# Kernel optimization log

Measured on AMD Instinct MI355X. Metric: run time of the kernel, lower is better.

The kernel has to match this reference:

```python
import jax, jax.numpy as jnp
import numpy as np

DIM = 2048
RANK = 16
NUM_EXPERTS = 8


def setup_inputs() -> dict:
    key = jax.random.key(0)
    ks = jax.random.split(key, 8)
    x = jax.random.normal(ks[0], (4, 2048, DIM), dtype=jnp.float32)
    # router gate: nn.Linear(dim, num_experts) -> weight [E, dim], bias [E]
    gate_w = jax.random.normal(ks[1], (NUM_EXPERTS, DIM), dtype=jnp.float32) * 0.02
    gate_b = jnp.zeros((NUM_EXPERTS,), dtype=jnp.float32)
    # base_ffn: nn.Linear(dim, dim) -> weight [dim, dim], bias [dim]
    base_w = jax.random.normal(ks[2], (DIM, DIM), dtype=jnp.float32) * 0.02
    base_b = jnp.zeros((DIM,), dtype=jnp.float32)
    # LoRA experts, stacked: A maps dim->rank, B maps rank->dim (stored input-major)
    lora_A = jax.random.normal(ks[3], (NUM_EXPERTS, DIM, RANK), dtype=jnp.float32) * 0.02
    lora_B = jax.random.normal(ks[4], (NUM_EXPERTS, RANK, DIM), dtype=jnp.float32) * 0.02
    return {"x": x, "gate_w": gate_w, "gate_b": gate_b,
            "base_w": base_w, "base_b": base_b,
            "lora_A": lora_A, "lora_B": lora_B}


def reference(x, gate_w, gate_b, base_w, base_b, lora_A, lora_B):
    B, S, D = x.shape
    flat = x.reshape(-1, D)  # [T, D]
    # base FFN: Linear + exact GELU (torch default)
    base_out = jax.nn.gelu(flat @ base_w.T + base_b, approximate=False)
    # router: softmax then top-1
    probs = jax.nn.softmax(flat @ gate_w.T + gate_b, axis=-1)  # [T, E]
    idx = jnp.argmax(probs, axis=-1)                            # [T] top-1 index
    w = jnp.take_along_axis(probs, idx[:, None], axis=-1)      # [T, 1] top-1 weight
    E = lora_A.shape[0]
    expert_out = jnp.zeros_like(flat)
    for e in range(E):  # fixed small expert loop; GEMMs are dense over all tokens
        h = jax.nn.gelu(flat @ lora_A[e], approximate=False)   # [T, rank]
        ye = h @ lora_B[e]                                      # [T, D]
        sel = (idx == e)[:, None]
        expert_out = expert_out + jnp.where(sel, ye * w, 0.0)
    out = (base_out + expert_out).reshape(B, S, D)
    return out, probs
```

## Files before the change

### kernel.cpp

```cpp
#include <hip/hip_runtime.h>
#include <hip/hip_bf16.h>
#include <math.h>


#define DIM   2048
#define RANK  16
#define NEXP  8
#define NTOK  8192
#define KLORA 128

typedef __hip_bfloat16 bf16;
typedef __attribute__((ext_vector_type(8))) short short8;
typedef __attribute__((ext_vector_type(4))) float float4v;

typedef const __attribute__((address_space(1))) void* gptr_t;
typedef __attribute__((address_space(3))) void*       sptr_t;

__device__ __forceinline__ void async_ld16(const bf16* g, bf16* l) {
    __builtin_amdgcn_global_load_lds((gptr_t)g, (sptr_t)l, 16, 0, 0);
}

__device__ __forceinline__ float gelu_fast(float x) {
    float t = 0.7978845608028654f * (x + 0.044715f * x * x * x);
    t = fminf(fmaxf(t, -10.0f), 10.0f);
    float e = __expf(2.0f * t);
    float th = (e - 1.0f) / (e + 1.0f);
    return 0.5f * x * (1.0f + th);
}

__device__ __forceinline__ short8 pack8(float4 v0, float4 v1) {
    union { bf16 h[8]; short8 v; } u;
    u.h[0] = __float2bfloat16(v0.x); u.h[1] = __float2bfloat16(v0.y);
    u.h[2] = __float2bfloat16(v0.z); u.h[3] = __float2bfloat16(v0.w);
    u.h[4] = __float2bfloat16(v1.x); u.h[5] = __float2bfloat16(v1.y);
    u.h[6] = __float2bfloat16(v1.z); u.h[7] = __float2bfloat16(v1.w);
    return u.v;
}

__global__ __launch_bounds__(256) void cvt_logits_kernel(
    const float* __restrict__ x, const float* __restrict__ gate_w,
    const float* __restrict__ gate_b, const float* __restrict__ base_w,
    const float* __restrict__ lora_B, const float* __restrict__ lora_A,
    bf16* __restrict__ Xb, bf16* __restrict__ Wb,
    bf16* __restrict__ Bt, bf16* __restrict__ Ab,
    float* __restrict__ probs, int* __restrict__ idx_out, float* __restrict__ w_out)
{
    __shared__ float buf[2560];
    const int b   = blockIdx.x;
    const int tid = threadIdx.x;

    if (b < 1024) {
        const int t0 = b * 8;
        float4 g0[NEXP], g1[NEXP];
        #pragma unroll
        for (int e = 0; e < NEXP; e++) {
            const float* wr = gate_w + (size_t)e * DIM + tid * 8;
            g0[e] = *(const float4*)wr;
            g1[e] = *(const float4*)(wr + 4);
        }
        const int wave = tid >> 6, lane = tid & 63;
        #pragma unroll
        for (int tt = 0; tt < 8; tt++) {
            const int t = t0 + tt;
            const float* xr = x + (size_t)t * DIM + tid * 8;
            float4 v0 = *(const float4*)xr;
            float4 v1 = *(const float4*)(xr + 4);
            *(short8*)(Xb + (size_t)t * DIM + tid * 8) = pack8(v0, v1);
            float a[NEXP];
            #pragma unroll
            for (int e = 0; e < NEXP; e++) {
                a[e] = v0.x * g0[e].x + v0.y * g0[e].y + v0.z * g0[e].z + v0.w * g0[e].w
                     + v1.x * g1[e].x + v1.y * g1[e].y + v1.z * g1[e].z + v1.w * g1[e].w;
                #pragma unroll
                for (int off = 32; off > 0; off >>= 1) a[e] += __shfl_down(a[e], off);
            }
            if (lane == 0) {
                #pragma unroll
                for (int e = 0; e < NEXP; e++) buf[tt * 32 + wave * NEXP + e] = a[e];
            }
        }
        __syncthreads();
        if (tid < 8) {
            const int t = t0 + tid;
            float l[NEXP]; float mx = -1e30f;
            #pragma unroll
            for (int e = 0; e < NEXP; e++) {
                l[e] = buf[tid * 32 + e] + buf[tid * 32 + 8 + e]
                     + buf[tid * 32 + 16 + e] + buf[tid * 32 + 24 + e] + gate_b[e];
                mx = fmaxf(mx, l[e]);
            }
            float sum = 0.f;
            #pragma unroll
            for (int e = 0; e < NEXP; e++) { l[e] = __expf(l[e] - mx); sum += l[e]; }
            float inv = 1.0f / sum;
            int es = 0; float best = l[0];
            #pragma unroll
            for (int e = 1; e < NEXP; e++) if (l[e] > best) { best = l[e]; es = e; }
            #pragma unroll
            for (int e = 0; e < NEXP; e++) probs[(size_t)t * NEXP + e] = l[e] * inv;
            idx_out[t] = es;
            w_out[t]   = best * inv;
        }
    } else if (b < 1024 + 2048) {
        size_t v = ((size_t)(b - 1024) * 256 + tid) * 8;
        float4 v0 = *(const float4*)(base_w + v);
        float4 v1 = *(const float4*)(base_w + v + 4);
        *(short8*)(Wb + v) = pack8(v0, v1);
    } else if (b < 1024 + 2048 + 256) {
        int bb = b - 1024 - 2048;
        int kk0 = (bb >> 6) * 32, j0 = (bb & 63) * 32;
        {
            int r = tid >> 3, c4 = (tid & 7) * 4;
            float4 val = *(const float4*)(lora_B + (size_t)(kk0 + r) * DIM + j0 + c4);
            *(float4*)(buf + r * 36 + c4) = val;
        }
        __syncthreads();
        {
            int j = tid >> 3, k4 = (tid & 7) * 4;
            bf16* dst = Bt + (size_t)(j0 + j) * KLORA + kk0 + k4;
            #pragma unroll
            for (int i = 0; i < 4; i++) dst[i] = __float2bfloat16(buf[(k4 + i) * 36 + j]);
        }
    } else {
        int bb = b - 1024 - 2048 - 256;
        int e = bb >> 4, k0 = (bb & 15) * 128;
        const float* src = lora_A + (size_t)e * DIM * RANK;
        {
            int k = tid >> 2, r4 = (tid & 3) * 4;
            float4 va = *(const float4*)(src + (size_t)(k0 + k) * RANK + r4);
            float4 vb = *(const float4*)(src + (size_t)(k0 + k + 64) * RANK + r4);
            *(float4*)(buf + k * 20 + r4)        = va;
            *(float4*)(buf + (k + 64) * 20 + r4) = vb;
        }
        __syncthreads();
        {
            int r = tid >> 4, kx = (tid & 15) * 8;
            bf16* dst = Ab + (size_t)(e * 16 + r) * DIM + k0 + kx;
            #pragma unroll
            for (int i = 0; i < 8; i++) dst[i] = __float2bfloat16(buf[(kx + i) * 20 + r]);
        }
    }
}

__global__ __launch_bounds__(256) void hsel_kernel(
    const bf16* __restrict__ Xb, const bf16* __restrict__ Ab,
    const int* __restrict__ idx, const float* __restrict__ wsel,
    bf16* __restrict__ A2)
{
    __shared__ bf16 As[32 * 32];
    __shared__ bf16 Bs[64 * 32];
    const int tid  = threadIdx.x;
    const int wave = tid >> 6, lane = tid & 63;
    const int m0 = blockIdx.x * 32;
    const int n0 = blockIdx.y * 64;
    const int col = lane & 15, quad = lane >> 4;

    const int kc = ((tid & 3) ^ ((tid >> 3) & 3)) * 8;
    const bf16* gB = Ab + (size_t)(n0 + (tid >> 2)) * DIM + kc;
    const bf16* gA = Xb + (size_t)(m0 + (tid >> 2)) * DIM + kc;
    bf16* lB = Bs + wave * 512;
    bf16* lA = As + wave * 512;

    const int xr = quad ^ ((col >> 1) & 3);
    const bf16* pa = As + col * 32 + xr * 8;
    const bf16* pb = Bs + (wave * 16 + col) * 32 + xr * 8;

    float4v acc[2] = {};
    for (int k0 = 0; k0 < DIM; k0 += 32) {
        __syncthreads();
        async_ld16(gB + k0, lB);
        if (tid < 128) async_ld16(gA + k0, lA);
        __syncthreads();
        short8 a0 = *(const short8*)pa;
        short8 a1 = *(const short8*)(pa + 512);
        short8 b0 = *(const short8*)pb;
        acc[0] = __builtin_amdgcn_mfma_f32_16x16x32_bf16(a0, b0, acc[0], 0, 0, 0);
        acc[1] = __builtin_amdgcn_mfma_f32_16x16x32_bf16(a1, b0, acc[1], 0, 0, 0);
    }

    const int jcol = n0 + wave * 16 + col;
    const int ej   = jcol >> 4;
    #pragma unroll
    for (int i = 0; i < 2; i++) {
        int rbase = m0 + i * 16 + quad * 4;
        #pragma unroll
        for (int r = 0; r < 4; r++) {
            int t = rbase + r;
            float v = (idx[t] == ej) ? gelu_fast(acc[i][r]) * wsel[t] : 0.0f;
            A2[(size_t)t * KLORA + jcol] = __float2bfloat16(v);
        }
    }
}

__global__ __launch_bounds__(256, 3) void gemm_kernel(
    const bf16* __restrict__ Xb, const bf16* __restrict__ Wb,
    const float* __restrict__ base_b,
    const bf16* __restrict__ A2, const bf16* __restrict__ Bt,
    float* __restrict__ out)
{
    __shared__ bf16 As[128 * 64];
    __shared__ bf16 Bs[128 * 64];
    const int tid  = threadIdx.x;
    const int wave = tid >> 6, lane = tid & 63;
    const int wm = wave >> 1, wn = wave & 1;
    const int n0 = blockIdx.x * 128;
    const int m0 = blockIdx.y * 128;
    const int col = lane & 15, quad = lane >> 4;

    const int kc = (((tid & 7) ^ ((tid >> 3) & 7))) * 8;
    const int r0 = tid >> 3;
    const bf16* gA0 = Xb + (size_t)(m0 + r0) * DIM + kc;
    const bf16* gB0 = Wb + (size_t)(n0 + r0) * DIM + kc;
    const bf16* gA1 = gA0 + (size_t)32 * DIM;
    const bf16* gB1 = gB0 + (size_t)32 * DIM;
    const bf16* gA2 = gA0 + (size_t)64 * DIM;
    const bf16* gB2 = gB0 + (size_t)64 * DIM;
    const bf16* gA3 = gA0 + (size_t)96 * DIM;
    const bf16* gB3 = gB0 + (size_t)96 * DIM;
    bf16* lA = As + wave * 512;
    bf16* lB = Bs + wave * 512;

    const int sl0 = (quad        ^ (col & 7)) * 8;
    const int sl1 = ((quad | 4)  ^ (col & 7)) * 8;
    const bf16* paA = As + (wm * 64 + col) * 64;
    const bf16* pbB = Bs + (wn * 64 + col) * 64;

    float4v acc[4][4] = {};

    for (int k0 = 0; k0 < DIM; k0 += 64) {
        __syncthreads();
        async_ld16(gA0 + k0, lA);
        async_ld16(gA1 + k0, lA + 2048);
        async_ld16(gA2 + k0, lA + 4096);
        async_ld16(gA3 + k0, lA + 6144);
        async_ld16(gB0 + k0, lB);
        async_ld16(gB1 + k0, lB + 2048);
        async_ld16(gB2 + k0, lB + 4096);
        async_ld16(gB3 + k0, lB + 6144);
        __syncthreads();
        {
            short8 a[4], b[4];
            #pragma unroll
            for (int i = 0; i < 4; i++) a[i] = *(const short8*)(paA + i * 1024 + sl0);
            #pragma unroll
            for (int j = 0; j < 4; j++) b[j] = *(const short8*)(pbB + j * 1024 + sl0);
            #pragma unroll
            for (int i = 0; i < 4; i++)
                #pragma unroll
                for (int j = 0; j < 4; j++)
                    acc[i][j] = __builtin_amdgcn_mfma_f32_16x16x32_bf16(
                        a[i], b[j], acc[i][j], 0, 0, 0);
        }
        {
            short8 a[4], b[4];
            #pragma unroll
            for (int i = 0; i < 4; i++) a[i] = *(const short8*)(paA + i * 1024 + sl1);
            #pragma unroll
            for (int j = 0; j < 4; j++) b[j] = *(const short8*)(pbB + j * 1024 + sl1);
            #pragma unroll
            for (int i = 0; i < 4; i++)
                #pragma unroll
                for (int j = 0; j < 4; j++)
                    acc[i][j] = __builtin_amdgcn_mfma_f32_16x16x32_bf16(
                        a[i], b[j], acc[i][j], 0, 0, 0);
        }
    }

    float bias[4];
    #pragma unroll
    for (int j = 0; j < 4; j++) bias[j] = base_b[n0 + wn * 64 + j * 16 + col];
    #pragma unroll
    for (int i = 0; i < 4; i++)
        #pragma unroll
        for (int j = 0; j < 4; j++)
            #pragma unroll
            for (int r = 0; r < 4; r++)
                acc[i][j][r] = gelu_fast(acc[i][j][r] + bias[j]);

    const bf16* pea = A2 + (size_t)(m0 + wm * 64 + col) * KLORA + quad * 8;
    const bf16* peb = Bt + (size_t)(n0 + wn * 64 + col) * KLORA + quad * 8;
    #pragma unroll
    for (int ks = 0; ks < 4; ks++) {
        short8 ea[4], eb[4];
        #pragma unroll
        for (int i = 0; i < 4; i++)
            ea[i] = *(const short8*)(pea + i * 16 * KLORA + ks * 32);
        #pragma unroll
        for (int j = 0; j < 4; j++)
            eb[j] = *(const short8*)(peb + j * 16 * KLORA + ks * 32);
        #pragma unroll
        for (int i = 0; i < 4; i++)
            #pragma unroll
            for (int j = 0; j < 4; j++)
                acc[i][j] = __builtin_amdgcn_mfma_f32_16x16x32_bf16(
                    ea[i], eb[j], acc[i][j], 0, 0, 0);
    }

    #pragma unroll
    for (int i = 0; i < 4; i++) {
        #pragma unroll
        for (int j = 0; j < 4; j++) {
            int tt = m0 + wm * 64 + i * 16 + quad * 4;
            int jj = n0 + wn * 64 + j * 16 + col;
            float* po = out + (size_t)tt * DIM + jj;
            #pragma unroll
            for (int r = 0; r < 4; r++) po[(size_t)r * DIM] = acc[i][j][r];
        }
    }
}

extern "C" void kernel_launch(void* const* d_in, const int* in_sizes, int n_in,
                              void* d_out, int out_size, void* d_ws, size_t ws_size,
                              hipStream_t stream)
{
    (void)in_sizes; (void)n_in; (void)out_size; (void)ws_size;
    const float* x      = (const float*)d_in[0];
    const float* gate_w = (const float*)d_in[1];
    const float* gate_b = (const float*)d_in[2];
    const float* base_w = (const float*)d_in[3];
    const float* base_b = (const float*)d_in[4];
    const float* lora_A = (const float*)d_in[5];
    const float* lora_B = (const float*)d_in[6];

    float* out   = (float*)d_out;
    float* probs = out + (size_t)NTOK * DIM;

    char* ws = (char*)d_ws;
    bf16*  Xb   = (bf16*)ws;
    bf16*  Wb   = (bf16*)(ws + 33554432);
    bf16*  A2   = (bf16*)(ws + 41943040);
    bf16*  Bt   = (bf16*)(ws + 44040192);
    bf16*  Ab   = (bf16*)(ws + 44564480);
    int*   idx  = (int*) (ws + 45088768);
    float* wsel = (float*)(ws + 45121536);

    cvt_logits_kernel<<<1024 + 2048 + 256 + 128, 256, 0, stream>>>(
        x, gate_w, gate_b, base_w, lora_B, lora_A,
        Xb, Wb, Bt, Ab, probs, idx, wsel);
    hsel_kernel<<<dim3(256, 2), 256, 0, stream>>>(Xb, Ab, idx, wsel, A2);
    gemm_kernel<<<dim3(16, 64), 256, 0, stream>>>(Xb, Wb, base_b, A2, Bt, out);
}
```

Baseline: 264.0 us.

## Enlarge GEMM tiles to 256x256 with 4-stage async LDS pipeline

Rewrites the main GEMM as 256x256 tiles with BK=32, 512 threads (8 waves) and a 4-deep ring of LDS buffers. Global-to-LDS async loads are issued three k-steps ahead and paced by explicit vmcnt waits, with MFMA bursts raised in priority via s_setprio. The aim is to hide global memory latency and raise arithmetic intensity per block. In exchange it uses more accumulator registers per wave and launches far fewer blocks (256), which risks poor CU load balance and register spills.

```diff
diff --git a/kernel.cpp b/kernel.cpp
--- a/kernel.cpp
+++ b/kernel.cpp
@@ -8,6 +8,12 @@
 #define NEXP  8
 #define NTOK  8192
 #define KLORA 128
+
+#define BM   256
+#define BN   256
+#define BK   32
+#define NBUF 4
+#define NKT  (DIM / BK)
 
 typedef __hip_bfloat16 bf16;
 typedef __attribute__((ext_vector_type(8))) short short8;
@@ -192,104 +198,126 @@
     }
 }
 
-__global__ __launch_bounds__(256, 3) void gemm_kernel(
+__global__ __launch_bounds__(512, 2) void gemm_kernel(
     const bf16* __restrict__ Xb, const bf16* __restrict__ Wb,
     const float* __restrict__ base_b,
     const bf16* __restrict__ A2, const bf16* __restrict__ Bt,
     float* __restrict__ out)
 {
-    __shared__ bf16 As[128 * 64];
-    __shared__ bf16 Bs[128 * 64];
+    __shared__ bf16 As[NBUF * BM * BK];
+    __shared__ bf16 Bs[NBUF * BN * BK];
     const int tid  = threadIdx.x;
     const int wave = tid >> 6, lane = tid & 63;
-    const int wm = wave >> 1, wn = wave & 1;
-    const int n0 = blockIdx.x * 128;
-    const int m0 = blockIdx.y * 128;
+    const int wm = wave >> 2, wn = wave & 3;
+    const int n0 = blockIdx.x * BN;
+    const int m0 = blockIdx.y * BM;
     const int col = lane & 15, quad = lane >> 4;
 
-    const int kc = (((tid & 7) ^ ((tid >> 3) & 7))) * 8;
-    const int r0 = tid >> 3;
-    const bf16* gA0 = Xb + (size_t)(m0 + r0) * DIM + kc;
-    const bf16* gB0 = Wb + (size_t)(n0 + r0) * DIM + kc;
-    const bf16* gA1 = gA0 + (size_t)32 * DIM;
-    const bf16* gB1 = gB0 + (size_t)32 * DIM;
-    const bf16* gA2 = gA0 + (size_t)64 * DIM;
-    const bf16* gB2 = gB0 + (size_t)64 * DIM;
-    const bf16* gA3 = gA0 + (size_t)96 * DIM;
-    const bf16* gB3 = gB0 + (size_t)96 * DIM;
-    bf16* lA = As + wave * 512;
-    bf16* lB = Bs + wave * 512;
-
-    const int sl0 = (quad        ^ (col & 7)) * 8;
-    const int sl1 = ((quad | 4)  ^ (col & 7)) * 8;
-    const bf16* paA = As + (wm * 64 + col) * 64;
-    const bf16* pbB = Bs + (wn * 64 + col) * 64;
-
-    float4v acc[4][4] = {};
-
-    for (int k0 = 0; k0 < DIM; k0 += 64) {
-        __syncthreads();
-        async_ld16(gA0 + k0, lA);
-        async_ld16(gA1 + k0, lA + 2048);
-        async_ld16(gA2 + k0, lA + 4096);
-        async_ld16(gA3 + k0, lA + 6144);
-        async_ld16(gB0 + k0, lB);
-        async_ld16(gB1 + k0, lB + 2048);
-        async_ld16(gB2 + k0, lB + 4096);
-        async_ld16(gB3 + k0, lB + 6144);
-        __syncthreads();
-        {
-            short8 a[4], b[4];
-            #pragma unroll
-            for (int i = 0; i < 4; i++) a[i] = *(const short8*)(paA + i * 1024 + sl0);
-            #pragma unroll
-            for (int j = 0; j < 4; j++) b[j] = *(const short8*)(pbB + j * 1024 + sl0);
-            #pragma unroll
-            for (int i = 0; i < 4; i++)
-                #pragma unroll
-                for (int j = 0; j < 4; j++)
-                    acc[i][j] = __builtin_amdgcn_mfma_f32_16x16x32_bf16(
-                        a[i], b[j], acc[i][j], 0, 0, 0);
-        }
-        {
-            short8 a[4], b[4];
-            #pragma unroll
-            for (int i = 0; i < 4; i++) a[i] = *(const short8*)(paA + i * 1024 + sl1);
-            #pragma unroll
-            for (int j = 0; j < 4; j++) b[j] = *(const short8*)(pbB + j * 1024 + sl1);
-            #pragma unroll
-            for (int i = 0; i < 4; i++)
-                #pragma unroll
-                for (int j = 0; j < 4; j++)
-                    acc[i][j] = __builtin_amdgcn_mfma_f32_16x16x32_bf16(
-                        a[i], b[j], acc[i][j], 0, 0, 0);
-        }
+    const int kc = ((tid & 3) ^ ((tid >> 3) & 3)) * 8;
+    const int sr = tid >> 2;
+    const bf16* gA = Xb + (size_t)(m0 + sr) * DIM + kc;
+    const bf16* gB = Wb + (size_t)(n0 + sr) * DIM + kc;
+    bf16* lAw = As + wave * 512;
+    bf16* lBw = Bs + wave * 512;
+
+    const int slot = (quad ^ ((col >> 1) & 3)) * 8;
+    const int raoff = (wm * 128 + col) * BK + slot;
+    const int rboff = (wn * 64  + col) * BK + slot;
+
+    float4v acc[8][4] = {};
+
+    #pragma unroll
+    for (int t = 0; t < 3; t++) {
+        const bf16* ga = gA + t * BK;
+        const bf16* gb = gB + t * BK;
+        bf16* la = lAw + t * (BM * BK);
+        bf16* lb = lBw + t * (BN * BK);
+        async_ld16(ga, la);
+        async_ld16(gb, lb);
+        async_ld16(ga + (size_t)128 * DIM, la + 4096);
+        async_ld16(gb + (size_t)128 * DIM, lb + 4096);
+    }
+    asm volatile("s_waitcnt vmcnt(8)" ::: "memory");
+    __builtin_amdgcn_sched_barrier(0);
+    __builtin_amdgcn_s_barrier();
+
+    #pragma unroll 4
+    for (int T = 0; T < NKT; T++) {
+        const int bufc = T & 3;
+        const bf16* pa = As + bufc * (BM * BK) + raoff;
+        const bf16* pb = Bs + bufc * (BN * BK) + rboff;
+        const int ts = T + 3, bufs = ts & 3;
+        const bool st = (ts < NKT);
+        const bf16* gsa = gA + ts * BK;
+        const bf16* gsb = gB + ts * BK;
+        bf16* lsa = lAw + bufs * (BM * BK);
+        bf16* lsb = lBw + bufs * (BN * BK);
+
+        short8 a[4], b[4];
+        #pragma unroll
+        for (int i = 0; i < 4; i++) a[i] = *(const short8*)(pa + i * 16 * BK);
+        #pragma unroll
+        for (int j = 0; j < 4; j++) b[j] = *(const short8*)(pb + j * 16 * BK);
+        if (st) {
+            async_ld16(gsa, lsa);
+            async_ld16(gsb, lsb);
+        }
+        __builtin_amdgcn_s_barrier();
+        __builtin_amdgcn_s_setprio(1);
+        #pragma unroll
+        for (int i = 0; i < 4; i++)
+            #pragma unroll
+            for (int j = 0; j < 4; j++)
+                acc[i][j] = __builtin_amdgcn_mfma_f32_16x16x32_bf16(
+                    a[i], b[j], acc[i][j], 0, 0, 0);
+        __builtin_amdgcn_s_setprio(0);
+        __builtin_amdgcn_s_barrier();
+        #pragma unroll
+        for (int i = 0; i < 4; i++) a[i] = *(const short8*)(pa + (i + 4) * 16 * BK);
+        if (st) {
+            async_ld16(gsa + (size_t)128 * DIM, lsa + 4096);
+            async_ld16(gsb + (size_t)128 * DIM, lsb + 4096);
+        }
+        __builtin_amdgcn_s_barrier();
+        __builtin_amdgcn_s_setprio(1);
+        #pragma unroll
+        for (int i = 0; i < 4; i++)
+            #pragma unroll
+            for (int j = 0; j < 4; j++)
+                acc[i + 4][j] = __builtin_amdgcn_mfma_f32_16x16x32_bf16(
+                    a[i], b[j], acc[i + 4][j], 0, 0, 0);
+        __builtin_amdgcn_s_setprio(0);
+        if (T + 3 < NKT)      asm volatile("s_waitcnt vmcnt(8)" ::: "memory");
+        else if (T + 3 == NKT) asm volatile("s_waitcnt vmcnt(4)" ::: "memory");
+        else                   asm volatile("s_waitcnt vmcnt(0)" ::: "memory");
+        __builtin_amdgcn_sched_barrier(0);
+        __builtin_amdgcn_s_barrier();
     }
 
     float bias[4];
     #pragma unroll
     for (int j = 0; j < 4; j++) bias[j] = base_b[n0 + wn * 64 + j * 16 + col];
     #pragma unroll
-    for (int i = 0; i < 4; i++)
+    for (int i = 0; i < 8; i++)
         #pragma unroll
         for (int j = 0; j < 4; j++)
             #pragma unroll
             for (int r = 0; r < 4; r++)
                 acc[i][j][r] = gelu_fast(acc[i][j][r] + bias[j]);
 
-    const bf16* pea = A2 + (size_t)(m0 + wm * 64 + col) * KLORA + quad * 8;
-    const bf16* peb = Bt + (size_t)(n0 + wn * 64 + col) * KLORA + quad * 8;
+    const bf16* pea = A2 + (size_t)(m0 + wm * 128 + col) * KLORA + quad * 8;
+    const bf16* peb = Bt + (size_t)(n0 + wn * 64  + col) * KLORA + quad * 8;
     #pragma unroll
     for (int ks = 0; ks < 4; ks++) {
-        short8 ea[4], eb[4];
-        #pragma unroll
-        for (int i = 0; i < 4; i++)
+        short8 ea[8], eb[4];
+        #pragma unroll
+        for (int i = 0; i < 8; i++)
             ea[i] = *(const short8*)(pea + i * 16 * KLORA + ks * 32);
         #pragma unroll
         for (int j = 0; j < 4; j++)
             eb[j] = *(const short8*)(peb + j * 16 * KLORA + ks * 32);
         #pragma unroll
-        for (int i = 0; i < 4; i++)
+        for (int i = 0; i < 8; i++)
             #pragma unroll
             for (int j = 0; j < 4; j++)
                 acc[i][j] = __builtin_amdgcn_mfma_f32_16x16x32_bf16(
@@ -297,11 +325,11 @@
     }
 
     #pragma unroll
-    for (int i = 0; i < 4; i++) {
+    for (int i = 0; i < 8; i++) {
         #pragma unroll
         for (int j = 0; j < 4; j++) {
-            int tt = m0 + wm * 64 + i * 16 + quad * 4;
-            int jj = n0 + wn * 64 + j * 16 + col;
+            int tt = m0 + wm * 128 + i * 16 + quad * 4;
+            int jj = n0 + wn * 64  + j * 16 + col;
             float* po = out + (size_t)tt * DIM + jj;
             #pragma unroll
             for (int r = 0; r < 4; r++) po[(size_t)r * DIM] = acc[i][j][r];
@@ -338,5 +366,5 @@
         x, gate_w, gate_b, base_w, lora_B, lora_A,
         Xb, Wb, Bt, Ab, probs, idx, wsel);
     hsel_kernel<<<dim3(256, 2), 256, 0, stream>>>(Xb, Ab, idx, wsel, A2);
-    gemm_kernel<<<dim3(16, 64), 256, 0, stream>>>(Xb, Wb, base_b, A2, Bt, out);
-}
+    gemm_kernel<<<dim3(8, 32), 512, 0, stream>>>(Xb, Wb, base_b, A2, Bt, out);
+}
```

Result: faster. 250.8 us (-5.0%).
